# Performance work log

Hardware: AMD Instinct MI355X
Metric: run time of the kernel (lower is better)

## Reference

```python
import jax, jax.numpy as jnp
import numpy as np


def setup_inputs() -> dict:
    key = jax.random.key(0)
    x = jax.random.normal(key, (4, 256, 256, 256), dtype=jnp.float32)
    return {"x": x}


def reference(x):
    # Inverse DWT (Haar-style): split channels into 4 groups, linearly
    # combine, then interleave rows/cols (depth-to-space with r=2).
    B, H, W, C = x.shape
    oc = C // 4
    x1 = x[..., 0 * oc:1 * oc] * 0.5
    x2 = x[..., 1 * oc:2 * oc] * 0.5
    x3 = x[..., 2 * oc:3 * oc] * 0.5
    x4 = x[..., 3 * oc:4 * oc] * 0.5
    h01 = x1 - x2 - x3 + x4  # -> out[2r,   2c]
    h02 = x1 + x2 - x3 - x4  # -> out[2r+1, 2c]
    h03 = x1 - x2 + x3 - x4  # -> out[2r,   2c+1]
    h04 = x1 + x2 + x3 + x4  # -> out[2r+1, 2c+1]
    # t[b,h,w,ri,c,ci]: ri indexes row offset, ci indexes col offset
    t = jnp.stack(
        [jnp.stack([h01, h03], axis=4), jnp.stack([h02, h04], axis=4)],
        axis=3,
    )  # (B, H, W, 2, C/4, 2)
    out = jnp.transpose(t, (0, 1, 3, 2, 5, 4)).reshape(B, 2 * H, 2 * W, oc)
    return out
```

## Files before the change

### kernel.cpp

```cpp
#include <hip/hip_runtime.h>


__global__ __launch_bounds__(256) void idwt_kernel(const float* __restrict__ x,
                                                   float* __restrict__ out) {
    const int tid = blockIdx.x * blockDim.x + threadIdx.x;
    const int c4  = tid & 15;
    const int pix = tid >> 4;
    const int w   = pix & 255;
    const int h   = (pix >> 8) & 255;
    const int b   = pix >> 16;

    const float4* __restrict__ xin =
        reinterpret_cast<const float4*>(x + (size_t)pix * 256) + c4;

    const float4 a1 = xin[0];
    const float4 a2 = xin[16];
    const float4 a3 = xin[32];
    const float4 a4 = xin[48];

    float4 h01, h02, h03, h04;
    {
        const float s = 0.5f;
#define COMB(F, e)                                                \
        F.e = s * (a1.e) ;                                        \
        h01.e = s*(a1.e - a2.e - a3.e + a4.e);                    \
        h02.e = s*(a1.e + a2.e - a3.e - a4.e);                    \
        h03.e = s*(a1.e - a2.e + a3.e - a4.e);                    \
        h04.e = s*(a1.e + a2.e + a3.e + a4.e);
#undef COMB
#define MIX(e)                                                    \
        h01.e = s*(a1.e - a2.e - a3.e + a4.e);                    \
        h02.e = s*(a1.e + a2.e - a3.e - a4.e);                    \
        h03.e = s*(a1.e - a2.e + a3.e - a4.e);                    \
        h04.e = s*(a1.e + a2.e + a3.e + a4.e);
        MIX(x) MIX(y) MIX(z) MIX(w)
#undef MIX
    }

    const int r0 = 2 * h;
    const int c0 = 2 * w;
    float4* __restrict__ o00 = reinterpret_cast<float4*>(
        out + (((size_t)b * 512 + r0) * 512 + c0) * 64) + c4;
    float4* __restrict__ o01 = o00 + 16;
    float4* __restrict__ o10 = reinterpret_cast<float4*>(
        out + (((size_t)b * 512 + r0 + 1) * 512 + c0) * 64) + c4;
    float4* __restrict__ o11 = o10 + 16;

    o00[0] = h01;
    o10[0] = h02;
    o01[0] = h03;
    o11[0] = h04;
}

extern "C" void kernel_launch(void* const* d_in, const int* in_sizes, int n_in,
                              void* d_out, int out_size, void* d_ws, size_t ws_size,
                              hipStream_t stream) {
    const float* x = (const float*)d_in[0];
    float* out = (float*)d_out;

    const int total_threads = 4 * 256 * 256 * 16;
    const int block = 256;
    const int grid = total_threads / block;
    idwt_kernel<<<grid, block, 0, stream>>>(x, out);
}
```

Baseline: 98.30 us.

## Split work per output column and use nontemporal loads and stores

Measured after the change: 85.67 us. -12.8%, faster.

```diff
diff --git a/kernel.cpp b/kernel.cpp
--- a/kernel.cpp
+++ b/kernel.cpp
@@ -1,55 +1,35 @@
 #include <hip/hip_runtime.h>
 
 
+typedef float f32x4 __attribute__((ext_vector_type(4)));
+
 __global__ __launch_bounds__(256) void idwt_kernel(const float* __restrict__ x,
                                                    float* __restrict__ out) {
-    const int tid = blockIdx.x * blockDim.x + threadIdx.x;
-    const int c4  = tid & 15;
-    const int pix = tid >> 4;
-    const int w   = pix & 255;
-    const int h   = (pix >> 8) & 255;
-    const int b   = pix >> 16;
+    const int t  = blockIdx.x * blockDim.x + threadIdx.x;
+    const int c4 = t & 15;
+    const int o  = (t >> 4) & 511;
+    const int h  = (t >> 13) & 255;
+    const int b  = t >> 21;
+    const int w  = o >> 1;
+    const float sc = (o & 1) ? 1.0f : -1.0f;
 
-    const float4* __restrict__ xin =
-        reinterpret_cast<const float4*>(x + (size_t)pix * 256) + c4;
+    const f32x4* __restrict__ xin = reinterpret_cast<const f32x4*>(
+        x + (size_t)(((b * 256 + h) * 256 + w)) * 256) + c4;
 
-    const float4 a1 = xin[0];
-    const float4 a2 = xin[16];
-    const float4 a3 = xin[32];
-    const float4 a4 = xin[48];
+    const f32x4 a1 = __builtin_nontemporal_load(xin + 0);
+    const f32x4 a2 = __builtin_nontemporal_load(xin + 16);
+    const f32x4 a3 = __builtin_nontemporal_load(xin + 32);
+    const f32x4 a4 = __builtin_nontemporal_load(xin + 48);
 
-    float4 h01, h02, h03, h04;
-    {
-        const float s = 0.5f;
-#define COMB(F, e)                                                \
-        F.e = s * (a1.e) ;                                        \
-        h01.e = s*(a1.e - a2.e - a3.e + a4.e);                    \
-        h02.e = s*(a1.e + a2.e - a3.e - a4.e);                    \
-        h03.e = s*(a1.e - a2.e + a3.e - a4.e);                    \
-        h04.e = s*(a1.e + a2.e + a3.e + a4.e);
-#undef COMB
-#define MIX(e)                                                    \
-        h01.e = s*(a1.e - a2.e - a3.e + a4.e);                    \
-        h02.e = s*(a1.e + a2.e - a3.e - a4.e);                    \
-        h03.e = s*(a1.e - a2.e + a3.e - a4.e);                    \
-        h04.e = s*(a1.e + a2.e + a3.e + a4.e);
-        MIX(x) MIX(y) MIX(z) MIX(w)
-#undef MIX
-    }
+    const f32x4 ev = 0.5f * ((a1 - a2) + sc * (a3 - a4));
+    const f32x4 od = 0.5f * ((a1 + a2) + sc * (a3 + a4));
 
-    const int r0 = 2 * h;
-    const int c0 = 2 * w;
-    float4* __restrict__ o00 = reinterpret_cast<float4*>(
-        out + (((size_t)b * 512 + r0) * 512 + c0) * 64) + c4;
-    float4* __restrict__ o01 = o00 + 16;
-    float4* __restrict__ o10 = reinterpret_cast<float4*>(
-        out + (((size_t)b * 512 + r0 + 1) * 512 + c0) * 64) + c4;
-    float4* __restrict__ o11 = o10 + 16;
+    const size_t row_even = ((size_t)(b * 512 + 2 * h) * 512) * 16;
+    f32x4* __restrict__ oe = reinterpret_cast<f32x4*>(out) + row_even + (o * 16 + c4);
+    f32x4* __restrict__ oo = oe + 512 * 16;
 
-    o00[0] = h01;
-    o10[0] = h02;
-    o01[0] = h03;
-    o11[0] = h04;
+    __builtin_nontemporal_store(ev, oe);
+    __builtin_nontemporal_store(od, oo);
 }
 
 extern "C" void kernel_launch(void* const* d_in, const int* in_sizes, int n_in,
@@ -58,7 +38,7 @@
     const float* x = (const float*)d_in[0];
     float* out = (float*)d_out;
 
-    const int total_threads = 4 * 256 * 256 * 16;
+    const int total_threads = 4 * 256 * 512 * 16;
     const int block = 256;
     const int grid = total_threads / block;
     idwt_kernel<<<grid, block, 0, stream>>>(x, out);
```
